# Performance work log

Measured on AMD Instinct MI355X. Metric: run time of the kernel, lower is better.

## Reference

```python
import jax, jax.numpy as jnp
import numpy as np

T, B, E, H = 2048, 2, 1024, 16
HD = E // H
EPS = 1e-5


def setup_inputs() -> dict:
    key = jax.random.key(0)
    k1, k2, k3 = jax.random.split(key, 3)
    bound_in = float(np.sqrt(6.0 / (3 * E + E)))   # xavier_uniform for [3E,E]
    bound_out = float(np.sqrt(6.0 / (E + E)))      # xavier_uniform for [E,E]
    return {
        "query": jax.random.normal(k1, (T, B, E), dtype=jnp.float32),
        "gamma": jnp.ones((E,), dtype=jnp.float32),
        "beta": jnp.zeros((E,), dtype=jnp.float32),
        "in_proj_weight": jax.random.uniform(k2, (3 * E, E), jnp.float32, -bound_in, bound_in),
        "out_proj_weight": jax.random.uniform(k3, (E, E), jnp.float32, -bound_out, bound_out),
    }


def reference(query, gamma, beta, in_proj_weight, out_proj_weight):
    # LayerNorm over channel dim
    mean = jnp.mean(query, axis=-1, keepdims=True)
    var = jnp.mean(jnp.square(query - mean), axis=-1, keepdims=True)
    ln = (query - mean) * jax.lax.rsqrt(var + EPS) * gamma + beta  # [T,B,E]

    # Fused QKV projection (no bias): qkv = ln @ W^T, W: [3E, E]
    qkv = jnp.einsum("tbe,fe->tbf", ln, in_proj_weight)  # [T,B,3E]
    q, k, v = jnp.split(qkv, 3, axis=-1)
    q = q.reshape(T, B, H, HD) * (HD ** -0.5)
    k = k.reshape(T, B, H, HD)
    v = v.reshape(T, B, H, HD)

    # Attention: scores [B,H,T,T]
    scores = jnp.einsum("tbhd,sbhd->bhts", q, k)
    attn = jax.nn.softmax(scores, axis=-1)
    ctx = jnp.einsum("bhts,sbhd->tbhd", attn, v).reshape(T, B, E)

    # Output projection + residual add (dropout prob = 0)
    out = jnp.einsum("tbe,fe->tbf", ctx, out_proj_weight)
    return query + out
```

## Files before the change

### kernel.cpp

```cpp
#include <hip/hip_runtime.h>
#include <hip/hip_bf16.h>
#include <math.h>

#define T_DIM 2048
#define B_DIM 2
#define E_DIM 1024
#define H_DIM 16
#define HD_DIM 64
#define M_DIM (T_DIM * B_DIM)
#define BH_DIM (B_DIM * H_DIM)

using bf16x8 = __attribute__((ext_vector_type(8))) __bf16;
using u16x8  = __attribute__((ext_vector_type(8))) unsigned short;
using u16x4  = __attribute__((ext_vector_type(4))) unsigned short;
using f32x4  = __attribute__((ext_vector_type(4))) float;

static __device__ __forceinline__ unsigned short f2bf(float f) {
  unsigned u = __builtin_bit_cast(unsigned, f);
  u += 0x7fff + ((u >> 16) & 1);
  return (unsigned short)(u >> 16);
}

__device__ __forceinline__ void gload_lds16(const void* g, void* l) {
  __builtin_amdgcn_global_load_lds(
      (const __attribute__((address_space(1))) unsigned int*)g,
      (__attribute__((address_space(3))) unsigned int*)l, 16, 0, 0);
}

__global__ __launch_bounds__(256) void cast2_kernel(
    const float* __restrict__ in1, unsigned short* __restrict__ out1, int n1,
    const float* __restrict__ in2, unsigned short* __restrict__ out2, int n2) {
  int i = blockIdx.x * 256 + threadIdx.x;
  const float* in; unsigned short* out; int idx;
  if (i < n1) { in = in1; out = out1; idx = i; }
  else if (i < n1 + n2) { in = in2; out = out2; idx = i - n1; }
  else return;
  float4 v = ((const float4*)in)[idx];
  ushort4 o;
  o.x = f2bf(v.x); o.y = f2bf(v.y); o.z = f2bf(v.z); o.w = f2bf(v.w);
  ((ushort4*)out)[idx] = o;
}

__global__ __launch_bounds__(256) void ln_kernel(
    const float* __restrict__ q, const float* __restrict__ gamma,
    const float* __restrict__ beta, unsigned short* __restrict__ out) {
  int row = blockIdx.x;
  int tid = threadIdx.x;
  const float4* qr = (const float4*)(q + (size_t)row * E_DIM);
  float4 x = qr[tid];
  float s  = x.x + x.y + x.z + x.w;
  float ss = x.x * x.x + x.y * x.y + x.z * x.z + x.w * x.w;
#pragma unroll
  for (int off = 32; off >= 1; off >>= 1) {
    s  += __shfl_xor(s, off, 64);
    ss += __shfl_xor(ss, off, 64);
  }
  __shared__ float red[8];
  int wid = tid >> 6, lane = tid & 63;
  if (lane == 0) { red[wid] = s; red[4 + wid] = ss; }
  __syncthreads();
  s  = red[0] + red[1] + red[2] + red[3];
  ss = red[4] + red[5] + red[6] + red[7];
  float mean = s * (1.0f / E_DIM);
  float var  = ss * (1.0f / E_DIM) - mean * mean;
  float rstd = rsqrtf(var + 1e-5f);
  float4 g4 = ((const float4*)gamma)[tid];
  float4 b4 = ((const float4*)beta)[tid];
  ushort4 o;
  o.x = f2bf((x.x - mean) * rstd * g4.x + b4.x);
  o.y = f2bf((x.y - mean) * rstd * g4.y + b4.y);
  o.z = f2bf((x.z - mean) * rstd * g4.z + b4.z);
  o.w = f2bf((x.w - mean) * rstd * g4.w + b4.w);
  ((ushort4*)(out + (size_t)row * E_DIM))[tid] = o;
}

__global__ __launch_bounds__(256) void gemm0_kernel(
    const unsigned short* __restrict__ A, const unsigned short* __restrict__ Bw,
    unsigned short* __restrict__ out_qkv) {
  __shared__ alignas(16) unsigned short lA[128 * 32];
  __shared__ alignas(16) unsigned short lB[128 * 32];
  int tid = threadIdx.x;
  int wid = tid >> 6, lane = tid & 63;
  int wm = wid >> 1, wn = wid & 1;
  int g = lane >> 4, lr = lane & 15;
  int m0 = blockIdx.y * 128, n0 = blockIdx.x * 128;
  f32x4 acc[4][4] = {};

  for (int k0 = 0; k0 < E_DIM; k0 += 32) {
#pragma unroll
    for (int c = 0; c < 2; ++c) {
      int f16 = c * 256 + tid;
      int row = f16 >> 2, col8 = (f16 & 3) << 3;
      gload_lds16(A  + (size_t)(m0 + row) * E_DIM + k0 + col8,
                  lA + (size_t)(c * 256 + wid * 64) * 8);
      gload_lds16(Bw + (size_t)(n0 + row) * E_DIM + k0 + col8,
                  lB + (size_t)(c * 256 + wid * 64) * 8);
    }
    __syncthreads();
    bf16x8 af[4], bfr[4];
#pragma unroll
    for (int r = 0; r < 4; ++r) {
      af[r]  = *(const bf16x8*)(lA + (wm * 64 + r * 16 + lr) * 32 + g * 8);
      bfr[r] = *(const bf16x8*)(lB + (wn * 64 + r * 16 + lr) * 32 + g * 8);
    }
#pragma unroll
    for (int mr = 0; mr < 4; ++mr)
#pragma unroll
      for (int nr = 0; nr < 4; ++nr)
        acc[mr][nr] = __builtin_amdgcn_mfma_f32_16x16x32_bf16(
            af[mr], bfr[nr], acc[mr][nr], 0, 0, 0);
    __syncthreads();
  }

#pragma unroll
  for (int mr = 0; mr < 4; ++mr) {
#pragma unroll
    for (int nr = 0; nr < 4; ++nr) {
#pragma unroll
      for (int r = 0; r < 4; ++r) {
        int grow = m0 + wm * 64 + mr * 16 + g * 4 + r;
        int gcol = n0 + wn * 64 + nr * 16 + lr;
        int which = gcol >> 10, rem = gcol & 1023;
        int h = rem >> 6, d = rem & 63;
        int t = grow >> 1, b = grow & 1;
        out_qkv[(size_t)which * (BH_DIM * T_DIM * HD_DIM) +
                ((size_t)(b * H_DIM + h) * T_DIM + t) * HD_DIM + d] =
            f2bf(acc[mr][nr][r]);
      }
    }
  }
}

__global__ __launch_bounds__(256) void gemm1_kernel(
    const unsigned short* __restrict__ A, const unsigned short* __restrict__ Bw,
    const float* __restrict__ resid, float* __restrict__ out) {
  __shared__ alignas(16) unsigned short lA[128 * 32];
  __shared__ alignas(16) unsigned short lB[64 * 32];
  int tid = threadIdx.x;
  int wid = tid >> 6, lane = tid & 63;
  int g = lane >> 4, lr = lane & 15;
  int m0 = blockIdx.y * 128, n0 = blockIdx.x * 64;
  f32x4 acc[2][4] = {};

  for (int k0 = 0; k0 < E_DIM; k0 += 32) {
#pragma unroll
    for (int c = 0; c < 2; ++c) {
      int f16 = c * 256 + tid;
      int row = f16 >> 2, col8 = (f16 & 3) << 3;
      gload_lds16(A + (size_t)(m0 + row) * E_DIM + k0 + col8,
                  lA + (size_t)(c * 256 + wid * 64) * 8);
    }
    {
      int row = tid >> 2, col8 = (tid & 3) << 3;
      gload_lds16(Bw + (size_t)(n0 + row) * E_DIM + k0 + col8,
                  lB + (size_t)(wid * 64) * 8);
    }
    __syncthreads();
    bf16x8 af[2], bfr[4];
#pragma unroll
    for (int r = 0; r < 2; ++r)
      af[r] = *(const bf16x8*)(lA + (wid * 32 + r * 16 + lr) * 32 + g * 8);
#pragma unroll
    for (int r = 0; r < 4; ++r)
      bfr[r] = *(const bf16x8*)(lB + (r * 16 + lr) * 32 + g * 8);
#pragma unroll
    for (int mr = 0; mr < 2; ++mr)
#pragma unroll
      for (int nr = 0; nr < 4; ++nr)
        acc[mr][nr] = __builtin_amdgcn_mfma_f32_16x16x32_bf16(
            af[mr], bfr[nr], acc[mr][nr], 0, 0, 0);
    __syncthreads();
  }

#pragma unroll
  for (int mr = 0; mr < 2; ++mr) {
#pragma unroll
    for (int nr = 0; nr < 4; ++nr) {
#pragma unroll
      for (int r = 0; r < 4; ++r) {
        int grow = m0 + wid * 32 + mr * 16 + g * 4 + r;
        int gcol = n0 + nr * 16 + lr;
        size_t idx = (size_t)grow * E_DIM + gcol;
        out[idx] = resid[idx] + acc[mr][nr][r];
      }
    }
  }
}

__global__ __launch_bounds__(256) void transpose_v_kernel(
    const unsigned short* __restrict__ vb, unsigned short* __restrict__ vt) {
  __shared__ alignas(16) unsigned short tl[64 * 72];
  int tid = threadIdx.x;
  int bh = blockIdx.y, t0 = blockIdx.x * 64;
  const unsigned short* src = vb + ((size_t)bh * T_DIM + t0) * HD_DIM;
#pragma unroll
  for (int e = 0; e < 2; ++e) {
    int i8 = e * 256 + tid;
    int r = i8 >> 3;
    int c = (i8 & 7) * 8;
    int hsh = (r ^ (r >> 3)) & 7;
    bf16x8 v = *(const bf16x8*)(src + (size_t)r * HD_DIM + c);
    *(bf16x8*)(tl + r * 72 + (c ^ (hsh << 3))) = v;
  }
  __syncthreads();
  unsigned short* dst = vt + (size_t)bh * HD_DIM * T_DIM + t0;
#pragma unroll
  for (int e = 0; e < 2; ++e) {
    int i8 = e * 256 + tid;
    int d = i8 >> 3;
    int tc = (i8 & 7) * 8;
    u16x8 o;
#pragma unroll
    for (int j = 0; j < 8; ++j) {
      int p = tc + j;
      int ks = p >> 5, gg = (p >> 3) & 3, jl = p & 7;
      int r = (ks * 2 + (jl >> 2)) * 16 + gg * 4 + (jl & 3);
      int hsh = (r ^ (r >> 3)) & 7;
      o[j] = tl[r * 72 + (d ^ (hsh << 3))];
    }
    *(u16x8*)(dst + (size_t)d * T_DIM + tc) = o;
  }
}

__global__ __launch_bounds__(256) void attn_kernel(
    const unsigned short* __restrict__ qb, const unsigned short* __restrict__ kb,
    const unsigned short* __restrict__ vt, unsigned short* __restrict__ ctx) {
  __shared__ alignas(16) unsigned short lK[3][64 * 64];
  __shared__ alignas(16) unsigned short lV[3][64 * 64];
  int tid = threadIdx.x;
  int wid = tid >> 6, lane = tid & 63;
  int g = lane >> 4, lr = lane & 15;
  int f = blockIdx.x;
  int xcd = f & 7, rest = f >> 3;
  int bh = xcd + 8 * (rest & 3);
  int qt = rest >> 2;
  int b = bh >> 4, h = bh & 15;
  const size_t koff = (size_t)bh * T_DIM * HD_DIM;
  const size_t voff = (size_t)bh * HD_DIM * T_DIM;

  int srow = tid >> 3;
  int gch  = (tid & 7) ^ (srow & 7);
  const unsigned short* ks0 = kb + koff + (size_t)srow * HD_DIM + gch * 8;
  const unsigned short* vs0 = vt + voff + (size_t)srow * T_DIM + gch * 8;

#define STAGE_TILE(buf, kofs, vofs)                                            \
  do {                                                                         \
    gload_lds16(ks0 + (kofs),                 lK[buf] + wid * 512);            \
    gload_lds16(ks0 + (kofs) + 32 * HD_DIM,   lK[buf] + 2048 + wid * 512);     \
    gload_lds16(vs0 + (vofs),                 lV[buf] + wid * 512);            \
    gload_lds16(vs0 + (vofs) + (size_t)32 * T_DIM, lV[buf] + 2048 + wid * 512);\
  } while (0)

  bf16x8 qf[2][2];
  {
    const float QS = 0.125f * 1.44269504f;
#pragma unroll
    for (int qa = 0; qa < 2; ++qa) {
      int qrow = qt * 128 + wid * 32 + qa * 16 + lr;
#pragma unroll
      for (int ks = 0; ks < 2; ++ks) {
        bf16x8 raw = *(const bf16x8*)(qb + koff + (size_t)qrow * HD_DIM + ks * 32 + g * 8);
#pragma unroll
        for (int j = 0; j < 8; ++j) qf[qa][ks][j] = (__bf16)((float)raw[j] * QS);
      }
    }
  }

  bf16x8 onesf;
#pragma unroll
  for (int j = 0; j < 8; ++j) onesf[j] = (__bf16)1.0f;

  f32x4 accO[2][4] = {};
  f32x4 accS[2] = {};

  const int NT = T_DIM / 64;
  STAGE_TILE(0, 0, 0);

#define PROCESS(BUF, NBUF, TT, LAST)                                           \
  do {                                                                         \
    if (!(LAST)) {                                                             \
      size_t s1 = (size_t)((TT) + 1) * 64;                                     \
      STAGE_TILE(NBUF, s1 * HD_DIM, s1);                                       \
      asm volatile("s_waitcnt vmcnt(4)" ::: "memory");                         \
    } else {                                                                   \
      asm volatile("s_waitcnt vmcnt(0)" ::: "memory");                         \
    }                                                                          \
    __builtin_amdgcn_s_barrier();                                              \
    __builtin_amdgcn_sched_barrier(0);                                         \
    const unsigned short* Kc = lK[BUF];                                        \
    const unsigned short* Vc = lV[BUF];                                        \
    f32x4 s4[2][4];                                                            \
    __builtin_amdgcn_s_setprio(1);                                             \
    _Pragma("unroll")                                                          \
    for (int cf = 0; cf < 4; ++cf) {                                           \
      int row = cf * 16 + lr;                                                  \
      int sw = (row & 7) << 3;                                                 \
      bf16x8 k0 = *(const bf16x8*)(Kc + row * 64 + ((g * 8) ^ sw));            \
      bf16x8 k1 = *(const bf16x8*)(Kc + row * 64 + ((32 + g * 8) ^ sw));       \
      _Pragma("unroll")                                                        \
      for (int qa = 0; qa < 2; ++qa) {                                         \
        f32x4 s = {-8.0f, -8.0f, -8.0f, -8.0f};                                \
        s = __builtin_amdgcn_mfma_f32_16x16x32_bf16(k0, qf[qa][0], s, 0, 0, 0);\
        s = __builtin_amdgcn_mfma_f32_16x16x32_bf16(k1, qf[qa][1], s, 0, 0, 0);\
        s4[qa][cf] = s;                                                        \
      }                                                                        \
    }                                                                          \
    __builtin_amdgcn_s_setprio(0);                                             \
    bf16x8 pf[2][2];                                                           \
    _Pragma("unroll")                                                          \
    for (int qa = 0; qa < 2; ++qa)                                             \
      _Pragma("unroll")                                                        \
      for (int j = 0; j < 8; ++j) {                                            \
        pf[qa][0][j] = (__bf16)__builtin_amdgcn_exp2f(s4[qa][(j >> 2)][j & 3]);\
        pf[qa][1][j] = (__bf16)__builtin_amdgcn_exp2f(s4[qa][2 + (j >> 2)][j & 3]);\
      }                                                                        \
    __builtin_amdgcn_s_setprio(1);                                             \
    _Pragma("unroll")                                                          \
    for (int ks = 0; ks < 2; ++ks) {                                           \
      _Pragma("unroll")                                                        \
      for (int qa = 0; qa < 2; ++qa)                                           \
        accS[qa] = __builtin_amdgcn_mfma_f32_16x16x32_bf16(onesf, pf[qa][ks], accS[qa], 0, 0, 0); \
      _Pragma("unroll")                                                        \
      for (int df = 0; df < 4; ++df) {                                         \
        int row = df * 16 + lr;                                                \
        int sw = (row & 7) << 3;                                               \
        bf16x8 vf = *(const bf16x8*)(Vc + row * 64 + ((ks * 32 + g * 8) ^ sw));\
        _Pragma("unroll")                                                      \
        for (int qa = 0; qa < 2; ++qa)                                         \
          accO[qa][df] = __builtin_amdgcn_mfma_f32_16x16x32_bf16(vf, pf[qa][ks], accO[qa][df], 0, 0, 0); \
      }                                                                        \
    }                                                                          \
    __builtin_amdgcn_s_setprio(0);                                             \
  } while (0)

  for (int t3 = 0; t3 < 30; t3 += 3) {
    PROCESS(0, 1, t3 + 0, false);
    PROCESS(1, 2, t3 + 1, false);
    PROCESS(2, 0, t3 + 2, false);
  }
  PROCESS(0, 1, 30, false);
  PROCESS(1, 2, 31, true);
#undef PROCESS
#undef STAGE_TILE

  __syncthreads();
  unsigned short* sc = (unsigned short*)lK + wid * (32 * 72);
  float invl[2];
  invl[0] = 1.0f / accS[0][0];
  invl[1] = 1.0f / accS[1][0];
#pragma unroll
  for (int qa = 0; qa < 2; ++qa)
#pragma unroll
    for (int df = 0; df < 4; ++df)
#pragma unroll
      for (int r = 0; r < 4; ++r)
        sc[(qa * 16 + lr) * 72 + df * 16 + g * 4 + r] =
            f2bf(accO[qa][df][r] * invl[qa]);
  __syncthreads();
#pragma unroll
  for (int i = 0; i < 4; ++i) {
    int idx = i * 64 + lane;
    int row = idx >> 3, ch = idx & 7;
    u16x8 v8 = *(const u16x8*)(sc + row * 72 + ch * 8);
    int t = qt * 128 + wid * 32 + row;
    *(u16x8*)(&ctx[((size_t)t * B_DIM + b) * E_DIM + h * HD_DIM + ch * 8]) = v8;
  }
}

extern "C" void kernel_launch(void* const* d_in, const int* in_sizes, int n_in,
                              void* d_out, int out_size, void* d_ws, size_t ws_size,
                              hipStream_t stream) {
  const float* query = (const float*)d_in[0];
  const float* gamma = (const float*)d_in[1];
  const float* beta  = (const float*)d_in[2];
  const float* w_in  = (const float*)d_in[3];
  const float* w_out = (const float*)d_in[4];
  float* out = (float*)d_out;

  unsigned short* ws    = (unsigned short*)d_ws;
  unsigned short* ln    = ws;
  unsigned short* winb  = ln + (size_t)M_DIM * E_DIM;
  unsigned short* woutb = winb + (size_t)3 * E_DIM * E_DIM;
  unsigned short* qkv   = woutb + (size_t)E_DIM * E_DIM;

  unsigned short* qbuf = qkv;
  unsigned short* kbuf = qkv + (size_t)BH_DIM * T_DIM * HD_DIM;
  unsigned short* vbuf = kbuf + (size_t)BH_DIM * T_DIM * HD_DIM;
  unsigned short* vtb  = ln;
  unsigned short* ctx  = vbuf;

  cast2_kernel<<<dim3(4096), dim3(256), 0, stream>>>(
      w_in, winb, 3 * E_DIM * E_DIM / 4, w_out, woutb, E_DIM * E_DIM / 4);
  ln_kernel<<<dim3(M_DIM), dim3(256), 0, stream>>>(query, gamma, beta, ln);
  gemm0_kernel<<<dim3(3 * E_DIM / 128, M_DIM / 128), dim3(256), 0, stream>>>(
      ln, winb, qkv);
  transpose_v_kernel<<<dim3(T_DIM / 64, BH_DIM), dim3(256), 0, stream>>>(vbuf, vtb);
  attn_kernel<<<dim3(512), dim3(256), 0, stream>>>(qbuf, kbuf, vtb, ctx);
  gemm1_kernel<<<dim3(E_DIM / 64, M_DIM / 128), dim3(256), 0, stream>>>(
      ctx, woutb, query, out);
}
```

Baseline: 122.3 us.

## Pipeline GEMM K-loops, restructure attention staging, fuse LN with weight cast

After: 122.2 us. About the same (-0.1%).

```diff
diff --git a/kernel.cpp b/kernel.cpp
--- a/kernel.cpp
+++ b/kernel.cpp
@@ -12,7 +12,6 @@
 
 using bf16x8 = __attribute__((ext_vector_type(8))) __bf16;
 using u16x8  = __attribute__((ext_vector_type(8))) unsigned short;
-using u16x4  = __attribute__((ext_vector_type(4))) unsigned short;
 using f32x4  = __attribute__((ext_vector_type(4))) float;
 
 static __device__ __forceinline__ unsigned short f2bf(float f) {
@@ -27,25 +26,26 @@
       (__attribute__((address_space(3))) unsigned int*)l, 16, 0, 0);
 }
 
-__global__ __launch_bounds__(256) void cast2_kernel(
-    const float* __restrict__ in1, unsigned short* __restrict__ out1, int n1,
-    const float* __restrict__ in2, unsigned short* __restrict__ out2, int n2) {
-  int i = blockIdx.x * 256 + threadIdx.x;
-  const float* in; unsigned short* out; int idx;
-  if (i < n1) { in = in1; out = out1; idx = i; }
-  else if (i < n1 + n2) { in = in2; out = out2; idx = i - n1; }
-  else return;
-  float4 v = ((const float4*)in)[idx];
-  ushort4 o;
-  o.x = f2bf(v.x); o.y = f2bf(v.y); o.z = f2bf(v.z); o.w = f2bf(v.w);
-  ((ushort4*)out)[idx] = o;
-}
-
-__global__ __launch_bounds__(256) void ln_kernel(
+__global__ __launch_bounds__(256) void prep_kernel(
     const float* __restrict__ q, const float* __restrict__ gamma,
-    const float* __restrict__ beta, unsigned short* __restrict__ out) {
-  int row = blockIdx.x;
+    const float* __restrict__ beta, unsigned short* __restrict__ ln_out,
+    const float* __restrict__ w1, unsigned short* __restrict__ o1, int n1,
+    const float* __restrict__ w2, unsigned short* __restrict__ o2, int n2) {
+  int blk = blockIdx.x;
   int tid = threadIdx.x;
+  if (blk >= M_DIM) {
+    int i = (blk - M_DIM) * 256 + tid;
+    const float* in; unsigned short* out; int idx;
+    if (i < n1) { in = w1; out = o1; idx = i; }
+    else if (i < n1 + n2) { in = w2; out = o2; idx = i - n1; }
+    else return;
+    float4 v = ((const float4*)in)[idx];
+    ushort4 o;
+    o.x = f2bf(v.x); o.y = f2bf(v.y); o.z = f2bf(v.z); o.w = f2bf(v.w);
+    ((ushort4*)out)[idx] = o;
+    return;
+  }
+  int row = blk;
   const float4* qr = (const float4*)(q + (size_t)row * E_DIM);
   float4 x = qr[tid];
   float s  = x.x + x.y + x.z + x.w;
@@ -71,14 +71,14 @@
   o.y = f2bf((x.y - mean) * rstd * g4.y + b4.y);
   o.z = f2bf((x.z - mean) * rstd * g4.z + b4.z);
   o.w = f2bf((x.w - mean) * rstd * g4.w + b4.w);
-  ((ushort4*)(out + (size_t)row * E_DIM))[tid] = o;
+  ((ushort4*)(ln_out + (size_t)row * E_DIM))[tid] = o;
 }
 
 __global__ __launch_bounds__(256) void gemm0_kernel(
     const unsigned short* __restrict__ A, const unsigned short* __restrict__ Bw,
     unsigned short* __restrict__ out_qkv) {
-  __shared__ alignas(16) unsigned short lA[128 * 32];
-  __shared__ alignas(16) unsigned short lB[128 * 32];
+  __shared__ alignas(16) unsigned short lA[3][128 * 32];
+  __shared__ alignas(16) unsigned short lB[3][128 * 32];
   int tid = threadIdx.x;
   int wid = tid >> 6, lane = tid & 63;
   int wm = wid >> 1, wn = wid & 1;
@@ -86,31 +86,55 @@
   int m0 = blockIdx.y * 128, n0 = blockIdx.x * 128;
   f32x4 acc[4][4] = {};
 
-  for (int k0 = 0; k0 < E_DIM; k0 += 32) {
-#pragma unroll
-    for (int c = 0; c < 2; ++c) {
-      int f16 = c * 256 + tid;
-      int row = f16 >> 2, col8 = (f16 & 3) << 3;
-      gload_lds16(A  + (size_t)(m0 + row) * E_DIM + k0 + col8,
-                  lA + (size_t)(c * 256 + wid * 64) * 8);
-      gload_lds16(Bw + (size_t)(n0 + row) * E_DIM + k0 + col8,
-                  lB + (size_t)(c * 256 + wid * 64) * 8);
-    }
-    __syncthreads();
-    bf16x8 af[4], bfr[4];
-#pragma unroll
-    for (int r = 0; r < 4; ++r) {
-      af[r]  = *(const bf16x8*)(lA + (wm * 64 + r * 16 + lr) * 32 + g * 8);
-      bfr[r] = *(const bf16x8*)(lB + (wn * 64 + r * 16 + lr) * 32 + g * 8);
-    }
-#pragma unroll
-    for (int mr = 0; mr < 4; ++mr)
-#pragma unroll
-      for (int nr = 0; nr < 4; ++nr)
-        acc[mr][nr] = __builtin_amdgcn_mfma_f32_16x16x32_bf16(
-            af[mr], bfr[nr], acc[mr][nr], 0, 0, 0);
-    __syncthreads();
-  }
+#define STAGE_G0(BUF, K0)                                                      \
+  do {                                                                         \
+    _Pragma("unroll")                                                          \
+    for (int c = 0; c < 2; ++c) {                                              \
+      int f16 = c * 256 + tid;                                                 \
+      int row = f16 >> 2, col8 = (f16 & 3) << 3;                               \
+      gload_lds16(A  + (size_t)(m0 + row) * E_DIM + (K0) + col8,               \
+                  lA[BUF] + (size_t)(c * 256 + wid * 64) * 8);                 \
+      gload_lds16(Bw + (size_t)(n0 + row) * E_DIM + (K0) + col8,               \
+                  lB[BUF] + (size_t)(c * 256 + wid * 64) * 8);                 \
+    }                                                                          \
+  } while (0)
+
+#define PROCG0(BUF, NBUF, KK, LAST)                                            \
+  do {                                                                         \
+    if (!(LAST)) {                                                             \
+      STAGE_G0(NBUF, ((KK) + 1) * 32);                                         \
+      asm volatile("s_waitcnt vmcnt(4)" ::: "memory");                         \
+    } else {                                                                   \
+      asm volatile("s_waitcnt vmcnt(0)" ::: "memory");                         \
+    }                                                                          \
+    __builtin_amdgcn_s_barrier();                                              \
+    __builtin_amdgcn_sched_barrier(0);                                         \
+    bf16x8 af[4], bfr[4];                                                      \
+    _Pragma("unroll")                                                          \
+    for (int r = 0; r < 4; ++r) {                                              \
+      af[r]  = *(const bf16x8*)(lA[BUF] + (wm * 64 + r * 16 + lr) * 32 + g * 8); \
+      bfr[r] = *(const bf16x8*)(lB[BUF] + (wn * 64 + r * 16 + lr) * 32 + g * 8); \
+    }                                                                          \
+    __builtin_amdgcn_s_setprio(1);                                             \
+    _Pragma("unroll")                                                          \
+    for (int mr = 0; mr < 4; ++mr)                                             \
+      _Pragma("unroll")                                                        \
+      for (int nr = 0; nr < 4; ++nr)                                           \
+        acc[mr][nr] = __builtin_amdgcn_mfma_f32_16x16x32_bf16(                 \
+            af[mr], bfr[nr], acc[mr][nr], 0, 0, 0);                            \
+    __builtin_amdgcn_s_setprio(0);                                             \
+  } while (0)
+
+  STAGE_G0(0, 0);
+  for (int kk = 0; kk < 30; kk += 3) {
+    PROCG0(0, 1, kk + 0, false);
+    PROCG0(1, 2, kk + 1, false);
+    PROCG0(2, 0, kk + 2, false);
+  }
+  PROCG0(0, 1, 30, false);
+  PROCG0(1, 2, 31, true);
+#undef PROCG0
+#undef STAGE_G0
 
 #pragma unroll
   for (int mr = 0; mr < 4; ++mr) {
@@ -134,43 +158,67 @@
 __global__ __launch_bounds__(256) void gemm1_kernel(
     const unsigned short* __restrict__ A, const unsigned short* __restrict__ Bw,
     const float* __restrict__ resid, float* __restrict__ out) {
-  __shared__ alignas(16) unsigned short lA[128 * 32];
-  __shared__ alignas(16) unsigned short lB[64 * 32];
+  __shared__ alignas(16) unsigned short lA[3][128 * 32];
+  __shared__ alignas(16) unsigned short lB[3][64 * 32];
   int tid = threadIdx.x;
   int wid = tid >> 6, lane = tid & 63;
   int g = lane >> 4, lr = lane & 15;
   int m0 = blockIdx.y * 128, n0 = blockIdx.x * 64;
   f32x4 acc[2][4] = {};
 
-  for (int k0 = 0; k0 < E_DIM; k0 += 32) {
-#pragma unroll
-    for (int c = 0; c < 2; ++c) {
-      int f16 = c * 256 + tid;
-      int row = f16 >> 2, col8 = (f16 & 3) << 3;
-      gload_lds16(A + (size_t)(m0 + row) * E_DIM + k0 + col8,
-                  lA + (size_t)(c * 256 + wid * 64) * 8);
-    }
-    {
-      int row = tid >> 2, col8 = (tid & 3) << 3;
-      gload_lds16(Bw + (size_t)(n0 + row) * E_DIM + k0 + col8,
-                  lB + (size_t)(wid * 64) * 8);
-    }
-    __syncthreads();
-    bf16x8 af[2], bfr[4];
-#pragma unroll
-    for (int r = 0; r < 2; ++r)
-      af[r] = *(const bf16x8*)(lA + (wid * 32 + r * 16 + lr) * 32 + g * 8);
-#pragma unroll
-    for (int r = 0; r < 4; ++r)
-      bfr[r] = *(const bf16x8*)(lB + (r * 16 + lr) * 32 + g * 8);
-#pragma unroll
-    for (int mr = 0; mr < 2; ++mr)
-#pragma unroll
-      for (int nr = 0; nr < 4; ++nr)
-        acc[mr][nr] = __builtin_amdgcn_mfma_f32_16x16x32_bf16(
-            af[mr], bfr[nr], acc[mr][nr], 0, 0, 0);
-    __syncthreads();
-  }
+#define STAGE_G1(BUF, K0)                                                      \
+  do {                                                                         \
+    _Pragma("unroll")                                                          \
+    for (int c = 0; c < 2; ++c) {                                              \
+      int f16 = c * 256 + tid;                                                 \
+      int row = f16 >> 2, col8 = (f16 & 3) << 3;                               \
+      gload_lds16(A + (size_t)(m0 + row) * E_DIM + (K0) + col8,                \
+                  lA[BUF] + (size_t)(c * 256 + wid * 64) * 8);                 \
+    }                                                                          \
+    {                                                                          \
+      int row = tid >> 2, col8 = (tid & 3) << 3;                               \
+      gload_lds16(Bw + (size_t)(n0 + row) * E_DIM + (K0) + col8,               \
+                  lB[BUF] + (size_t)(wid * 64) * 8);                           \
+    }                                                                          \
+  } while (0)
+
+#define PROCG1(BUF, NBUF, KK, LAST)                                            \
+  do {                                                                         \
+    if (!(LAST)) {                                                             \
+      STAGE_G1(NBUF, ((KK) + 1) * 32);                                         \
+      asm volatile("s_waitcnt vmcnt(3)" ::: "memory");                         \
+    } else {                                                                   \
+      asm volatile("s_waitcnt vmcnt(0)" ::: "memory");                         \
+    }                                                                          \
+    __builtin_amdgcn_s_barrier();                                              \
+    __builtin_amdgcn_sched_barrier(0);                                         \
+    bf16x8 af[2], bfr[4];                                                      \
+    _Pragma("unroll")                                                          \
+    for (int r = 0; r < 2; ++r)                                                \
+      af[r] = *(const bf16x8*)(lA[BUF] + (wid * 32 + r * 16 + lr) * 32 + g * 8); \
+    _Pragma("unroll")                                                          \
+    for (int r = 0; r < 4; ++r)                                                \
+      bfr[r] = *(const bf16x8*)(lB[BUF] + (r * 16 + lr) * 32 + g * 8);         \
+    __builtin_amdgcn_s_setprio(1);                                             \
+    _Pragma("unroll")                                                          \
+    for (int mr = 0; mr < 2; ++mr)                                             \
+      _Pragma("unroll")                                                        \
+      for (int nr = 0; nr < 4; ++nr)                                           \
+        acc[mr][nr] = __builtin_amdgcn_mfma_f32_16x16x32_bf16(                 \
+            af[mr], bfr[nr], acc[mr][nr], 0, 0, 0);                            \
+    __builtin_amdgcn_s_setprio(0);                                             \
+  } while (0)
+
+  STAGE_G1(0, 0);
+  for (int kk = 0; kk < 30; kk += 3) {
+    PROCG1(0, 1, kk + 0, false);
+    PROCG1(1, 2, kk + 1, false);
+    PROCG1(2, 0, kk + 2, false);
+  }
+  PROCG1(0, 1, 30, false);
+  PROCG1(1, 2, 31, true);
+#undef PROCG1
+#undef STAGE_G1
 
 #pragma unroll
   for (int mr = 0; mr < 2; ++mr) {
@@ -225,8 +273,8 @@
 __global__ __launch_bounds__(256) void attn_kernel(
     const unsigned short* __restrict__ qb, const unsigned short* __restrict__ kb,
     const unsigned short* __restrict__ vt, unsigned short* __restrict__ ctx) {
-  __shared__ alignas(16) unsigned short lK[3][64 * 64];
-  __shared__ alignas(16) unsigned short lV[3][64 * 64];
+  __shared__ alignas(16) unsigned short lK[4][64 * 64];
+  __shared__ alignas(16) unsigned short lV[4][64 * 64];
   int tid = threadIdx.x;
   int wid = tid >> 6, lane = tid & 63;
   int g = lane >> 4, lr = lane & 15;
@@ -243,12 +291,14 @@
   const unsigned short* ks0 = kb + koff + (size_t)srow * HD_DIM + gch * 8;
   const unsigned short* vs0 = vt + voff + (size_t)srow * T_DIM + gch * 8;
 
-#define STAGE_TILE(buf, kofs, vofs)                                            \
-  do {                                                                         \
-    gload_lds16(ks0 + (kofs),                 lK[buf] + wid * 512);            \
-    gload_lds16(ks0 + (kofs) + 32 * HD_DIM,   lK[buf] + 2048 + wid * 512);     \
-    gload_lds16(vs0 + (vofs),                 lV[buf] + wid * 512);            \
-    gload_lds16(vs0 + (vofs) + (size_t)32 * T_DIM, lV[buf] + 2048 + wid * 512);\
+#define STAGE_TILE(buf, T)                                                     \
+  do {                                                                         \
+    size_t kofs = (size_t)(T) * 64 * HD_DIM;                                   \
+    size_t vofs = (size_t)(T) * 64;                                            \
+    gload_lds16(ks0 + kofs,                 lK[buf] + wid * 512);              \
+    gload_lds16(ks0 + kofs + 32 * HD_DIM,   lK[buf] + 2048 + wid * 512);       \
+    gload_lds16(vs0 + vofs,                 lV[buf] + wid * 512);              \
+    gload_lds16(vs0 + vofs + (size_t)32 * T_DIM, lV[buf] + 2048 + wid * 512);  \
   } while (0)
 
   bf16x8 qf[2][2];
@@ -273,22 +323,10 @@
   f32x4 accO[2][4] = {};
   f32x4 accS[2] = {};
 
-  const int NT = T_DIM / 64;
-  STAGE_TILE(0, 0, 0);
-
-#define PROCESS(BUF, NBUF, TT, LAST)                                           \
-  do {                                                                         \
-    if (!(LAST)) {                                                             \
-      size_t s1 = (size_t)((TT) + 1) * 64;                                     \
-      STAGE_TILE(NBUF, s1 * HD_DIM, s1);                                       \
-      asm volatile("s_waitcnt vmcnt(4)" ::: "memory");                         \
-    } else {                                                                   \
-      asm volatile("s_waitcnt vmcnt(0)" ::: "memory");                         \
-    }                                                                          \
-    __builtin_amdgcn_s_barrier();                                              \
-    __builtin_amdgcn_sched_barrier(0);                                         \
-    const unsigned short* Kc = lK[BUF];                                        \
-    const unsigned short* Vc = lV[BUF];                                        \
+#define COMPUTE_TILE(B)                                                        \
+  do {                                                                         \
+    const unsigned short* Kc = lK[B];                                          \
+    const unsigned short* Vc = lV[B];                                          \
     f32x4 s4[2][4];                                                            \
     __builtin_amdgcn_s_setprio(1);                                             \
     _Pragma("unroll")                                                          \
@@ -333,14 +371,29 @@
     __builtin_amdgcn_s_setprio(0);                                             \
   } while (0)
 
-  for (int t3 = 0; t3 < 30; t3 += 3) {
-    PROCESS(0, 1, t3 + 0, false);
-    PROCESS(1, 2, t3 + 1, false);
-    PROCESS(2, 0, t3 + 2, false);
-  }
-  PROCESS(0, 1, 30, false);
-  PROCESS(1, 2, 31, true);
-#undef PROCESS
+#define INTERVAL(BA, BB, SA, SB, TT, STG)                                      \
+  do {                                                                         \
+    asm volatile("s_waitcnt vmcnt(0)" ::: "memory");                           \
+    __builtin_amdgcn_s_barrier();                                              \
+    __builtin_amdgcn_sched_barrier(0);                                         \
+    if (STG) {                                                                 \
+      STAGE_TILE(SA, (TT) + 2);                                                \
+      STAGE_TILE(SB, (TT) + 3);                                                \
+    }                                                                          \
+    COMPUTE_TILE(BA);                                                          \
+    COMPUTE_TILE(BB);                                                          \
+  } while (0)
+
+  STAGE_TILE(0, 0);
+  STAGE_TILE(1, 1);
+  for (int tt = 0; tt < 28; tt += 4) {
+    INTERVAL(0, 1, 2, 3, tt, true);
+    INTERVAL(2, 3, 0, 1, tt + 2, true);
+  }
+  INTERVAL(0, 1, 2, 3, 28, true);
+  INTERVAL(2, 3, 0, 1, 30, false);
+#undef INTERVAL
+#undef COMPUTE_TILE
 #undef STAGE_TILE
 
   __syncthreads();
@@ -389,9 +442,9 @@
   unsigned short* vtb  = ln;
   unsigned short* ctx  = vbuf;
 
-  cast2_kernel<<<dim3(4096), dim3(256), 0, stream>>>(
+  prep_kernel<<<dim3(M_DIM + 4096), dim3(256), 0, stream>>>(
+      query, gamma, beta, ln,
       w_in, winb, 3 * E_DIM * E_DIM / 4, w_out, woutb, E_DIM * E_DIM / 4);
-  ln_kernel<<<dim3(M_DIM), dim3(256), 0, stream>>>(query, gamma, beta, ln);
   gemm0_kernel<<<dim3(3 * E_DIM / 128, M_DIM / 128), dim3(256), 0, stream>>>(
       ln, winb, qkv);
   transpose_v_kernel<<<dim3(T_DIM / 64, BH_DIM), dim3(256), 0, stream>>>(vbuf, vtb);
```
